# Kernel optimization log

Hardware: AMD Instinct MI355X
Metric: run time of the kernel (lower is better)

Reference implementation:

```python
import jax, jax.numpy as jnp
import numpy as np

T, B, E, H = 2048, 2, 1024, 16
D = E // H  # head_dim = 64

def setup_inputs() -> dict:
    key = jax.random.key(0)
    ks = jax.random.split(key, 9)
    s = 1.0 / np.sqrt(E)
    return {
        "query": jax.random.normal(ks[0], (T, B, E), dtype=jnp.float32),
        "Wq": jax.random.normal(ks[1], (E, E), dtype=jnp.float32) * s,
        "bq": jax.random.normal(ks[2], (E,), dtype=jnp.float32) * 0.02,
        "Wk": jax.random.normal(ks[3], (E, E), dtype=jnp.float32) * s,
        "bk": jax.random.normal(ks[4], (E,), dtype=jnp.float32) * 0.02,
        "Wv": jax.random.normal(ks[5], (E, E), dtype=jnp.float32) * s,
        "bv": jax.random.normal(ks[6], (E,), dtype=jnp.float32) * 0.02,
        "Wo": jax.random.normal(ks[7], (E, E), dtype=jnp.float32) * s,
        "bo": jax.random.normal(ks[8], (E,), dtype=jnp.float32) * 0.02,
    }

def reference(query, Wq, bq, Wk, bk, Wv, bv, Wo, bo):
    # query: [T, B, E] (fairseq Time x Batch x Channel layout)
    t, b, e = query.shape
    scaling = D ** -0.5
    q = (query @ Wq.T + bq) * scaling          # [T,B,E], scaled like fairseq
    k = query @ Wk.T + bk                      # self-attention: k,v from query
    v = query @ Wv.T + bv
    # split heads: [T,B,H,D]
    q = q.reshape(t, b, H, D)
    k = k.reshape(t, b, H, D)
    v = v.reshape(t, b, H, D)
    # attn weights: [B,H,T(tgt),S(src)]
    scores = jnp.einsum("tbhd,sbhd->bhts", q, k)
    probs = jax.nn.softmax(scores, axis=-1)
    # attend: [T,B,H,D] -> [T,B,E]
    ctx = jnp.einsum("bhts,sbhd->tbhd", probs, v).reshape(t, b, e)
    return ctx @ Wo.T + bo                     # [T,B,E]
```

## Files before the change

kernel.cpp:

```cpp
#include <hip/hip_runtime.h>
#include <hip/hip_bf16.h>
#include <math.h>

#define TT 2048
#define BB 2
#define EE 1024
#define HH 16
#define DD 64
#define RR (TT*BB)

typedef __bf16 bf16x8 __attribute__((ext_vector_type(8)));
typedef float  floatx4 __attribute__((ext_vector_type(4)));

__device__ __forceinline__ unsigned short f2b(float f) {
    union { float f; unsigned u; } x{f};
    return (unsigned short)((x.u + 0x7FFFu + ((x.u >> 16) & 1u)) >> 16);
}
__device__ __forceinline__ float b2f_lo(unsigned u) {
    union { unsigned u; float f; } x{u << 16}; return x.f;
}
__device__ __forceinline__ float b2f_hi(unsigned u) {
    union { unsigned u; float f; } x{u & 0xffff0000u}; return x.f;
}

__device__ __forceinline__ float exp2_fast(float x) {
    return __builtin_amdgcn_exp2f(x);
}

typedef const __attribute__((address_space(1))) unsigned int as1_u32;
typedef __attribute__((address_space(3))) unsigned int as3_u32;
__device__ __forceinline__ void gload16(const void* g, void* l) {
    __builtin_amdgcn_global_load_lds((as1_u32*)g, (as3_u32*)l, 16, 0, 0);
}

#define SCALE_Q 0.18033688011112042f

__device__ __forceinline__ int swz(int r) {
    return (r & 7) ^ (((r >> 3) & 3) << 1);
}

__global__ __launch_bounds__(256)
void pack_bf16(const float* __restrict__ x,  const float* __restrict__ wq,
               const float* __restrict__ wk, const float* __restrict__ wv,
               const float* __restrict__ wo, unsigned short* __restrict__ base,
               unsigned short* __restrict__ wob)
{
    const size_t M4 = (size_t)4 << 20, M7 = (size_t)7 << 20;
    const size_t e0 = ((size_t)blockIdx.x * 256 + threadIdx.x) * 8;
    const float* src;
    unsigned short* dst;
    if (e0 < M4) {
        src = x + e0; dst = base + e0;
    } else if (e0 < M7) {
        const int seg = (int)((e0 >> 20) - 4);
        const float* wsrc[3] = {wq, wk, wv};
        src = wsrc[seg] + (e0 & ((1u << 20) - 1));
        dst = base + e0;
    } else {
        src = wo + (e0 - M7); dst = wob + (e0 - M7);
    }
    const float4 a = *(const float4*)src;
    const float4 b = *(const float4*)(src + 4);
    union { unsigned short u[8]; uint4 v; } p;
    p.u[0] = f2b(a.x); p.u[1] = f2b(a.y); p.u[2] = f2b(a.z); p.u[3] = f2b(a.w);
    p.u[4] = f2b(b.x); p.u[5] = f2b(b.y); p.u[6] = f2b(b.z); p.u[7] = f2b(b.w);
    *(uint4*)dst = p.v;
}

template<int MODE>
__global__ __launch_bounds__(256)
void gemm_mfma(const unsigned short* __restrict__ A,
               const unsigned short* __restrict__ Bw,
               const float* __restrict__ b0, const float* __restrict__ b1,
               const float* __restrict__ b2,
               void* __restrict__ out0, void* __restrict__ out1,
               void* __restrict__ out2)
{
    constexpr int BM = 128;
    constexpr int BN = (MODE == 0) ? 128 : 64;
    constexpr int MT = 4;
    constexpr int NT = (MODE == 0) ? 4 : 2;
    constexpr int RA = BM / 32;
    constexpr int RB = BN / 32;
    constexpr int ABYTES = BM * 128;
    constexpr int BUFB   = (BM + BN) * 128;
    __shared__ __align__(16) unsigned char smem[2 * BUFB];

    const int tid  = threadIdx.x;
    const int w    = tid >> 6;
    const int lane = tid & 63;
    const int quad = lane >> 4;
    const int l15  = lane & 15;
    const int wm   = w & 1;
    const int wn   = w >> 1;
    const int i0   = blockIdx.x * BM;
    const int j0   = blockIdx.y * BN;

    const unsigned short* ga[RA];
    const unsigned short* gb[RB];
    #pragma unroll
    for (int r = 0; r < RA; ++r) {
        const int slot = r * 256 + tid;
        const int row  = slot >> 3;
        const int gc   = (slot & 7) ^ swz(row);
        ga[r] = A + (size_t)(i0 + row) * EE + gc * 8;
    }
    #pragma unroll
    for (int r = 0; r < RB; ++r) {
        const int slot = r * 256 + tid;
        const int row  = slot >> 3;
        const int gc   = (slot & 7) ^ swz(row);
        gb[r] = Bw + (size_t)(j0 + row) * EE + gc * 8;
    }

    int ofsA[2][MT], ofsB[2][NT];
    #pragma unroll
    for (int mt = 0; mt < MT; ++mt) {
        const int row = wm * 64 + mt * 16 + l15;
        #pragma unroll
        for (int ks = 0; ks < 2; ++ks)
            ofsA[ks][mt] = row * 64 + (((ks * 4 + quad) ^ swz(row)) << 3);
    }
    #pragma unroll
    for (int nt = 0; nt < NT; ++nt) {
        const int col = wn * (BN / 2) + nt * 16 + l15;
        #pragma unroll
        for (int ks = 0; ks < 2; ++ks)
            ofsB[ks][nt] = col * 64 + (((ks * 4 + quad) ^ swz(col)) << 3);
    }

    floatx4 acc[MT][NT];
    #pragma unroll
    for (int mt = 0; mt < MT; ++mt)
        #pragma unroll
        for (int nt = 0; nt < NT; ++nt)
            acc[mt][nt] = (floatx4){0.f, 0.f, 0.f, 0.f};

    {
        unsigned short* nA = (unsigned short*)(smem);
        unsigned short* nB = (unsigned short*)(smem + ABYTES);
        #pragma unroll
        for (int r = 0; r < RA; ++r)
            gload16(ga[r], nA + (r * 256 + w * 64) * 8);
        #pragma unroll
        for (int r = 0; r < RB; ++r)
            gload16(gb[r], nB + (r * 256 + w * 64) * 8);
    }

    int cur = 0;
    for (int kk = 0; kk < EE; kk += 64) {
        __syncthreads();

        const unsigned short* lA = (const unsigned short*)(smem + cur * BUFB);
        const unsigned short* lB = (const unsigned short*)(smem + cur * BUFB + ABYTES);

        bf16x8 af[2][MT], bfr[2][NT];
        #pragma unroll
        for (int ks = 0; ks < 2; ++ks) {
            #pragma unroll
            for (int mt = 0; mt < MT; ++mt)
                af[ks][mt] = __builtin_bit_cast(bf16x8, *(const uint4*)&lA[ofsA[ks][mt]]);
            #pragma unroll
            for (int nt = 0; nt < NT; ++nt)
                bfr[ks][nt] = __builtin_bit_cast(bf16x8, *(const uint4*)&lB[ofsB[ks][nt]]);
        }

        if (kk + 64 < EE) {
            const int nxt = cur ^ 1;
            unsigned short* nA = (unsigned short*)(smem + nxt * BUFB);
            unsigned short* nB = (unsigned short*)(smem + nxt * BUFB + ABYTES);
            #pragma unroll
            for (int r = 0; r < RA; ++r)
                gload16(ga[r] + kk + 64, nA + (r * 256 + w * 64) * 8);
            #pragma unroll
            for (int r = 0; r < RB; ++r)
                gload16(gb[r] + kk + 64, nB + (r * 256 + w * 64) * 8);
        }
        __builtin_amdgcn_sched_barrier(0);

        #pragma unroll
        for (int ks = 0; ks < 2; ++ks)
            #pragma unroll
            for (int mt = 0; mt < MT; ++mt)
                #pragma unroll
                for (int nt = 0; nt < NT; ++nt)
                    acc[mt][nt] = __builtin_amdgcn_mfma_f32_16x16x32_bf16(
                        af[ks][mt], bfr[ks][nt], acc[mt][nt], 0, 0, 0);

        cur ^= 1;
    }

    if (MODE == 1) {
        float* dst = (float*)out0;
        #pragma unroll
        for (int nt = 0; nt < NT; ++nt) {
            const int j = j0 + wn * 32 + nt * 16 + l15;
            const float bb = b0[j];
            #pragma unroll
            for (int mt = 0; mt < MT; ++mt) {
                const int i = i0 + wm * 64 + mt * 16 + quad * 4;
                #pragma unroll
                for (int r2 = 0; r2 < 4; ++r2)
                    dst[(size_t)(i + r2) * EE + j] = acc[mt][nt][r2] + bb;
            }
        }
    } else {
        const int which = j0 >> 10;
        const float scale = (which == 0) ? SCALE_Q : 1.0f;
        const float* bias = (which == 0) ? b0 : (which == 1) ? b1 : b2;
        if (which < 2) {
            unsigned short* dst = (unsigned short*)(which == 0 ? out0 : out1);
            #pragma unroll
            for (int nt = 0; nt < NT; ++nt) {
                const int j = (j0 & 1023) + wn * 64 + nt * 16 + l15;
                const int h = j >> 6, d = j & 63;
                const float bb = bias[j];
                #pragma unroll
                for (int mt = 0; mt < MT; ++mt) {
                    const int i = i0 + wm * 64 + mt * 16 + quad * 4;
                    #pragma unroll
                    for (int r2 = 0; r2 < 4; ++r2) {
                        const int ii = i + r2;
                        const int t = ii >> 1, b = ii & 1;
                        dst[((size_t)(b * HH + h) * TT + t) * DD + d] =
                            f2b((acc[mt][nt][r2] + bb) * scale);
                    }
                }
            }
        } else {
            __syncthreads();
            unsigned short* tr = (unsigned short*)smem + (size_t)w * 64 * 68;
            #pragma unroll
            for (int nt = 0; nt < NT; ++nt) {
                const int jl = nt * 16 + l15;
                const float bb = bias[(j0 & 1023) + wn * 64 + jl];
                #pragma unroll
                for (int mt = 0; mt < MT; ++mt) {
                    const int il0 = mt * 16 + quad * 4;
                    ushort4 h4;
                    h4.x = f2b(acc[mt][nt][0] + bb);
                    h4.y = f2b(acc[mt][nt][1] + bb);
                    h4.z = f2b(acc[mt][nt][2] + bb);
                    h4.w = f2b(acc[mt][nt][3] + bb);
                    *(ushort4*)&tr[jl * 68 + il0] = h4;
                }
            }
            __syncthreads();
            const int jg = (j0 & 1023) + wn * 64 + lane;
            const int h = jg >> 6, d = jg & 63;
            const int tb = (i0 + wm * 64) >> 1;
            const unsigned short* rp = tr + (size_t)lane * 68;
            unsigned short* dstV = (unsigned short*)out2;
            #pragma unroll
            for (int g = 0; g < 4; ++g) {
                union { unsigned short u[8]; uint4 v; } pe, po;
                #pragma unroll
                for (int k = 0; k < 8; ++k) {
                    pe.u[k] = rp[(g * 8 + k) * 2];
                    po.u[k] = rp[(g * 8 + k) * 2 + 1];
                }
                *(uint4*)&dstV[((size_t)(0 * HH + h) * DD + d) * TT + tb + g * 8] = pe.v;
                *(uint4*)&dstV[((size_t)(1 * HH + h) * DD + d) * TT + tb + g * 8] = po.v;
            }
        }
    }
}

__global__ __launch_bounds__(256)
void attn_mfma(const unsigned short* __restrict__ Q,
               const unsigned short* __restrict__ K,
               const unsigned short* __restrict__ Vt,
               unsigned short* __restrict__ cpart,
               float* __restrict__ lsumbuf)
{
    __shared__ __align__(16) unsigned short ksm[2][64 * 64];
    __shared__ __align__(16) unsigned short vtm[2][64 * 64];

    const int tid  = threadIdx.x;
    const int w    = tid >> 6;
    const int lane = tid & 63;
    const int quad = lane >> 4;
    const int l15  = lane & 15;
    const int bh   = blockIdx.x;
    const int tt   = blockIdx.y;
    const int half = blockIdx.z;

    const unsigned short* Qh = Q  + (size_t)bh * TT * DD;
    const unsigned short* Kh = K  + (size_t)bh * TT * DD;
    const unsigned short* Vh = Vt + (size_t)bh * DD * TT;

    const int q0w  = tt * 128 + w * 32;
    const int key0 = half * 1024;

    bf16x8 qf[2][2];
    #pragma unroll
    for (int qn = 0; qn < 2; ++qn)
        #pragma unroll
        for (int kd = 0; kd < 2; ++kd)
            qf[qn][kd] = __builtin_bit_cast(bf16x8,
                *(const uint4*)&Qh[(size_t)(q0w + qn * 16 + l15) * DD + kd * 32 + quad * 8]);

    const unsigned short* kg[4];
    #pragma unroll
    for (int r = 0; r < 4; ++r) {
        const int slot = r * 256 + tid;
        const int row  = slot >> 3;
        const int gc   = (slot & 7) ^ swz(row);
        kg[r] = Kh + (size_t)(key0 + row) * DD + gc * 8;
    }
    const unsigned short* vg[4];
    #pragma unroll
    for (int r = 0; r < 4; ++r) {
        const int s512 = (r & 1) * 256 + tid;
        const int rowd = s512 >> 3;
        const int gc   = (s512 & 7) ^ swz(rowd);
        vg[r] = Vh + (size_t)rowd * TT + key0 + (r >> 1) * 64 + gc * 8;
    }

    int ofsKA[4][2], ofsVB[4][2];
    #pragma unroll
    for (int mt = 0; mt < 4; ++mt) {
        const int row = ((mt >> 1) << 5) + ((l15 >> 2) << 3) + ((mt & 1) << 2) + (l15 & 3);
        #pragma unroll
        for (int kd = 0; kd < 2; ++kd)
            ofsKA[mt][kd] = row * 64 + (((kd * 4 + quad) ^ swz(row)) << 3);
    }
    #pragma unroll
    for (int dn = 0; dn < 4; ++dn) {
        const int row = dn * 16 + l15;
        #pragma unroll
        for (int ks = 0; ks < 2; ++ks)
            ofsVB[dn][ks] = row * 64 + (((ks * 4 + quad) ^ swz(row)) << 3);
    }

    floatx4 cacc[4][2];
    #pragma unroll
    for (int dn = 0; dn < 4; ++dn)
        #pragma unroll
        for (int qn = 0; qn < 2; ++qn)
            cacc[dn][qn] = (floatx4){0.f, 0.f, 0.f, 0.f};
    float rs[2] = {0.f, 0.f};

    for (int big = 0; big < 8; ++big) {
        const size_t ko = (size_t)big * 128;
        __syncthreads();
        gload16(kg[0] + ko * DD, &ksm[0][(size_t)(0 * 256 + w * 64) * 8]);
        gload16(kg[1] + ko * DD, &ksm[0][(size_t)(1 * 256 + w * 64) * 8]);
        gload16(kg[2] + ko * DD, &ksm[1][(size_t)(0 * 256 + w * 64) * 8]);
        gload16(kg[3] + ko * DD, &ksm[1][(size_t)(1 * 256 + w * 64) * 8]);
        gload16(vg[0] + ko,      &vtm[0][(size_t)(0 * 256 + w * 64) * 8]);
        gload16(vg[1] + ko,      &vtm[0][(size_t)(1 * 256 + w * 64) * 8]);
        gload16(vg[2] + ko,      &vtm[1][(size_t)(0 * 256 + w * 64) * 8]);
        gload16(vg[3] + ko,      &vtm[1][(size_t)(1 * 256 + w * 64) * 8]);
        __syncthreads();

        #pragma unroll
        for (int sub = 0; sub < 2; ++sub) {
            uint2 pk[4][2];
            #pragma unroll
            for (int mt = 0; mt < 4; ++mt) {
                const bf16x8 ka0 = __builtin_bit_cast(bf16x8, *(const uint4*)&ksm[sub][ofsKA[mt][0]]);
                const bf16x8 ka1 = __builtin_bit_cast(bf16x8, *(const uint4*)&ksm[sub][ofsKA[mt][1]]);
                #pragma unroll
                for (int qn = 0; qn < 2; ++qn) {
                    floatx4 s = (floatx4){0.f, 0.f, 0.f, 0.f};
                    s = __builtin_amdgcn_mfma_f32_16x16x32_bf16(ka0, qf[qn][0], s, 0, 0, 0);
                    s = __builtin_amdgcn_mfma_f32_16x16x32_bf16(ka1, qf[qn][1], s, 0, 0, 0);
                    const float p0 = exp2_fast(s[0]);
                    const float p1 = exp2_fast(s[1]);
                    const float p2 = exp2_fast(s[2]);
                    const float p3 = exp2_fast(s[3]);
                    rs[qn] += (p0 + p1) + (p2 + p3);
                    union { __hip_bfloat162 h2[2]; uint2 u; } c;
                    c.h2[0] = __float22bfloat162_rn(make_float2(p0, p1));
                    c.h2[1] = __float22bfloat162_rn(make_float2(p2, p3));
                    pk[mt][qn] = c.u;
                }
            }
            bf16x8 pa[2][2];
            #pragma unroll
            for (int qn = 0; qn < 2; ++qn) {
                union { uint2 d[2]; uint4 v; } a0, a1;
                a0.d[0] = pk[0][qn]; a0.d[1] = pk[1][qn];
                a1.d[0] = pk[2][qn]; a1.d[1] = pk[3][qn];
                pa[qn][0] = __builtin_bit_cast(bf16x8, a0.v);
                pa[qn][1] = __builtin_bit_cast(bf16x8, a1.v);
            }
            #pragma unroll
            for (int dn = 0; dn < 4; ++dn) {
                const bf16x8 vb0 = __builtin_bit_cast(bf16x8, *(const uint4*)&vtm[sub][ofsVB[dn][0]]);
                const bf16x8 vb1 = __builtin_bit_cast(bf16x8, *(const uint4*)&vtm[sub][ofsVB[dn][1]]);
                #pragma unroll
                for (int qn = 0; qn < 2; ++qn) {
                    cacc[dn][qn] = __builtin_amdgcn_mfma_f32_16x16x32_bf16(pa[qn][0], vb0, cacc[dn][qn], 0, 0, 0);
                    cacc[dn][qn] = __builtin_amdgcn_mfma_f32_16x16x32_bf16(pa[qn][1], vb1, cacc[dn][qn], 0, 0, 0);
                }
            }
        }
    }

    const int b = bh / HH, hh = bh % HH;
    float rsw[2];
    #pragma unroll
    for (int qn = 0; qn < 2; ++qn) {
        float t = rs[qn];
        t += __shfl_xor(t, 16);
        t += __shfl_xor(t, 32);
        rsw[qn] = t;
    }
    unsigned short* cp = cpart + (size_t)half * RR * EE;
    #pragma unroll
    for (int qn = 0; qn < 2; ++qn) {
        #pragma unroll
        for (int dn = 0; dn < 4; ++dn) {
            const int e = hh * 64 + dn * 16 + l15;
            #pragma unroll
            for (int j = 0; j < 4; ++j) {
                const int t = q0w + qn * 16 + quad * 4 + j;
                cp[(size_t)(t * BB + b) * EE + e] = f2b(cacc[dn][qn][j]);
            }
        }
    }
    if (quad == 0) {
        lsumbuf[(half * BB * HH + bh) * TT + q0w + 0 * 16 + l15] = rsw[0];
        lsumbuf[(half * BB * HH + bh) * TT + q0w + 1 * 16 + l15] = rsw[1];
    }
}

__global__ __launch_bounds__(256)
void combine(const unsigned short* __restrict__ cpart,
             const float* __restrict__ lsumbuf,
             unsigned short* __restrict__ cb)
{
    const int gid = blockIdx.x * 256 + threadIdx.x;
    const int e0 = (gid & 127) * 8;
    const int r  = gid >> 7;
    const int t = r >> 1, b = r & 1;
    const int h = e0 >> 6;
    const int bh = b * HH + h;
    const float inv = 1.0f /
        (lsumbuf[bh * TT + t] + lsumbuf[(BB * HH + bh) * TT + t]);
    const uint4 c0 = *(const uint4*)&cpart[(size_t)r * EE + e0];
    const uint4 c1 = *(const uint4*)&cpart[(size_t)RR * EE + (size_t)r * EE + e0];
    const unsigned u0[4] = {c0.x, c0.y, c0.z, c0.w};
    const unsigned u1[4] = {c1.x, c1.y, c1.z, c1.w};
    union { unsigned u[4]; uint4 v; } o;
    #pragma unroll
    for (int k = 0; k < 4; ++k) {
        const float lo = (b2f_lo(u0[k]) + b2f_lo(u1[k])) * inv;
        const float hi = (b2f_hi(u0[k]) + b2f_hi(u1[k])) * inv;
        union { __hip_bfloat162 h2; unsigned u; } pk;
        pk.h2 = __float22bfloat162_rn(make_float2(lo, hi));
        o.u[k] = pk.u;
    }
    *(uint4*)&cb[(size_t)r * EE + e0] = o.v;
}

extern "C" void kernel_launch(void* const* d_in, const int* in_sizes, int n_in,
                              void* d_out, int out_size, void* d_ws, size_t ws_size,
                              hipStream_t stream)
{
    const float* x  = (const float*)d_in[0];
    const float* Wq = (const float*)d_in[1];
    const float* bq = (const float*)d_in[2];
    const float* Wk = (const float*)d_in[3];
    const float* bk = (const float*)d_in[4];
    const float* Wv = (const float*)d_in[5];
    const float* bv = (const float*)d_in[6];
    const float* Wo = (const float*)d_in[7];
    const float* bo = (const float*)d_in[8];
    float* out = (float*)d_out;

    const size_t M1 = (size_t)1 << 20;
    unsigned short* base  = (unsigned short*)d_ws;
    unsigned short* xb    = base;
    unsigned short* wqkv  = base + 4 * M1;
    unsigned short* cpart = base;
    unsigned short* qb    = base + 8 * M1;
    unsigned short* kb    = base + 12 * M1;
    unsigned short* vtb   = base + 16 * M1;
    unsigned short* cb    = base + 20 * M1;
    unsigned short* wob   = base + 24 * M1;
    float*          lsum  = (float*)(base + 25 * M1);

    dim3 blk(256);

    pack_bf16<<<dim3(4096), blk, 0, stream>>>(x, Wq, Wk, Wv, Wo, base, wob);

    gemm_mfma<0><<<dim3(RR / 128, 3072 / 128), blk, 0, stream>>>(
        xb, wqkv, bq, bk, bv, qb, kb, vtb);

    attn_mfma<<<dim3(BB * HH, TT / 128, 2), blk, 0, stream>>>(qb, kb, vtb, cpart, lsum);

    combine<<<dim3(RR * EE / 8 / 256), blk, 0, stream>>>(cpart, lsum, cb);

    gemm_mfma<1><<<dim3(RR / 128, EE / 64), blk, 0, stream>>>(
        cb, wob, bo, nullptr, nullptr, out, nullptr, nullptr);
}
```

Measured before the change: 189.5 us.

## Pipeline attention K/V loads with a three-stage LDS ring and reorder GEMM prefetch

The attention kernel previously loaded each 128-key K/V chunk synchronously between two barriers, so global-to-LDS latency was fully exposed. It now uses a three-buffer LDS ring with 64-key stages, issuing loads two stages ahead and waiting with vmcnt-based partial waits before one barrier per step. The GEMM loop also moves its next-tile prefetch ahead of the LDS fragment reads, using an explicit vmcnt(0) wait plus s_barrier. The ring raises LDS use by half, which may lower occupancy, and the hand-counted vmcnt values depend on gload16 issuing exactly one memory op each.

Result: faster. 179.7 us (-5.2%).

```diff
diff --git a/kernel.cpp b/kernel.cpp
--- a/kernel.cpp
+++ b/kernel.cpp
@@ -149,7 +149,20 @@
 
     int cur = 0;
     for (int kk = 0; kk < EE; kk += 64) {
-        __syncthreads();
+        asm volatile("s_waitcnt vmcnt(0)" ::: "memory");
+        __builtin_amdgcn_s_barrier();
+
+        if (kk + 64 < EE) {
+            unsigned short* nA = (unsigned short*)(smem + (cur ^ 1) * BUFB);
+            unsigned short* nB = (unsigned short*)(smem + (cur ^ 1) * BUFB + ABYTES);
+            #pragma unroll
+            for (int r = 0; r < RA; ++r)
+                gload16(ga[r] + kk + 64, nA + (r * 256 + w * 64) * 8);
+            #pragma unroll
+            for (int r = 0; r < RB; ++r)
+                gload16(gb[r] + kk + 64, nB + (r * 256 + w * 64) * 8);
+        }
+        __builtin_amdgcn_sched_barrier(0);
 
         const unsigned short* lA = (const unsigned short*)(smem + cur * BUFB);
         const unsigned short* lB = (const unsigned short*)(smem + cur * BUFB + ABYTES);
@@ -164,19 +177,6 @@
             for (int nt = 0; nt < NT; ++nt)
                 bfr[ks][nt] = __builtin_bit_cast(bf16x8, *(const uint4*)&lB[ofsB[ks][nt]]);
         }
-
-        if (kk + 64 < EE) {
-            const int nxt = cur ^ 1;
-            unsigned short* nA = (unsigned short*)(smem + nxt * BUFB);
-            unsigned short* nB = (unsigned short*)(smem + nxt * BUFB + ABYTES);
-            #pragma unroll
-            for (int r = 0; r < RA; ++r)
-                gload16(ga[r] + kk + 64, nA + (r * 256 + w * 64) * 8);
-            #pragma unroll
-            for (int r = 0; r < RB; ++r)
-                gload16(gb[r] + kk + 64, nB + (r * 256 + w * 64) * 8);
-        }
-        __builtin_amdgcn_sched_barrier(0);
 
         #pragma unroll
         for (int ks = 0; ks < 2; ++ks)
@@ -273,8 +273,7 @@
                unsigned short* __restrict__ cpart,
                float* __restrict__ lsumbuf)
 {
-    __shared__ __align__(16) unsigned short ksm[2][64 * 64];
-    __shared__ __align__(16) unsigned short vtm[2][64 * 64];
+    __shared__ __align__(16) unsigned short ring[3][2][64 * 64];
 
     const int tid  = threadIdx.x;
     const int w    = tid >> 6;
@@ -341,63 +340,74 @@
             cacc[dn][qn] = (floatx4){0.f, 0.f, 0.f, 0.f};
     float rs[2] = {0.f, 0.f};
 
-    for (int big = 0; big < 8; ++big) {
-        const size_t ko = (size_t)big * 128;
-        __syncthreads();
-        gload16(kg[0] + ko * DD, &ksm[0][(size_t)(0 * 256 + w * 64) * 8]);
-        gload16(kg[1] + ko * DD, &ksm[0][(size_t)(1 * 256 + w * 64) * 8]);
-        gload16(kg[2] + ko * DD, &ksm[1][(size_t)(0 * 256 + w * 64) * 8]);
-        gload16(kg[3] + ko * DD, &ksm[1][(size_t)(1 * 256 + w * 64) * 8]);
-        gload16(vg[0] + ko,      &vtm[0][(size_t)(0 * 256 + w * 64) * 8]);
-        gload16(vg[1] + ko,      &vtm[0][(size_t)(1 * 256 + w * 64) * 8]);
-        gload16(vg[2] + ko,      &vtm[1][(size_t)(0 * 256 + w * 64) * 8]);
-        gload16(vg[3] + ko,      &vtm[1][(size_t)(1 * 256 + w * 64) * 8]);
-        __syncthreads();
-
-        #pragma unroll
-        for (int sub = 0; sub < 2; ++sub) {
-            uint2 pk[4][2];
-            #pragma unroll
-            for (int mt = 0; mt < 4; ++mt) {
-                const bf16x8 ka0 = __builtin_bit_cast(bf16x8, *(const uint4*)&ksm[sub][ofsKA[mt][0]]);
-                const bf16x8 ka1 = __builtin_bit_cast(bf16x8, *(const uint4*)&ksm[sub][ofsKA[mt][1]]);
-                #pragma unroll
-                for (int qn = 0; qn < 2; ++qn) {
-                    floatx4 s = (floatx4){0.f, 0.f, 0.f, 0.f};
-                    s = __builtin_amdgcn_mfma_f32_16x16x32_bf16(ka0, qf[qn][0], s, 0, 0, 0);
-                    s = __builtin_amdgcn_mfma_f32_16x16x32_bf16(ka1, qf[qn][1], s, 0, 0, 0);
-                    const float p0 = exp2_fast(s[0]);
-                    const float p1 = exp2_fast(s[1]);
-                    const float p2 = exp2_fast(s[2]);
-                    const float p3 = exp2_fast(s[3]);
-                    rs[qn] += (p0 + p1) + (p2 + p3);
-                    union { __hip_bfloat162 h2[2]; uint2 u; } c;
-                    c.h2[0] = __float22bfloat162_rn(make_float2(p0, p1));
-                    c.h2[1] = __float22bfloat162_rn(make_float2(p2, p3));
-                    pk[mt][qn] = c.u;
-                }
-            }
-            bf16x8 pa[2][2];
+#define STAGE_ATTN(s)  do {                                                     \
+        const int p_ = (s) & 1;                                                 \
+        const size_t ko_ = (size_t)((s) >> 1) * 128;                            \
+        unsigned short* kd_ = &ring[(s) % 3][0][0];                             \
+        unsigned short* vd_ = &ring[(s) % 3][1][0];                             \
+        gload16(kg[2 * p_]     + ko_ * DD, kd_ + (size_t)(0 * 256 + w * 64) * 8); \
+        gload16(kg[2 * p_ + 1] + ko_ * DD, kd_ + (size_t)(1 * 256 + w * 64) * 8); \
+        gload16(vg[2 * p_]     + ko_,      vd_ + (size_t)(0 * 256 + w * 64) * 8); \
+        gload16(vg[2 * p_ + 1] + ko_,      vd_ + (size_t)(1 * 256 + w * 64) * 8); \
+    } while (0)
+
+    STAGE_ATTN(0);
+    STAGE_ATTN(1);
+
+    #pragma unroll
+    for (int step = 0; step < 16; ++step) {
+        const int rb = step % 3;
+        if (step < 15) asm volatile("s_waitcnt vmcnt(4)" ::: "memory");
+        else           asm volatile("s_waitcnt vmcnt(0)" ::: "memory");
+        __builtin_amdgcn_s_barrier();
+        if (step + 2 < 16) STAGE_ATTN(step + 2);
+        __builtin_amdgcn_sched_barrier(0);
+
+        const unsigned short* ksub = &ring[rb][0][0];
+        const unsigned short* vsub = &ring[rb][1][0];
+
+        uint2 pk[4][2];
+        #pragma unroll
+        for (int mt = 0; mt < 4; ++mt) {
+            const bf16x8 ka0 = __builtin_bit_cast(bf16x8, *(const uint4*)&ksub[ofsKA[mt][0]]);
+            const bf16x8 ka1 = __builtin_bit_cast(bf16x8, *(const uint4*)&ksub[ofsKA[mt][1]]);
             #pragma unroll
             for (int qn = 0; qn < 2; ++qn) {
-                union { uint2 d[2]; uint4 v; } a0, a1;
-                a0.d[0] = pk[0][qn]; a0.d[1] = pk[1][qn];
-                a1.d[0] = pk[2][qn]; a1.d[1] = pk[3][qn];
-                pa[qn][0] = __builtin_bit_cast(bf16x8, a0.v);
-                pa[qn][1] = __builtin_bit_cast(bf16x8, a1.v);
-            }
-            #pragma unroll
-            for (int dn = 0; dn < 4; ++dn) {
-                const bf16x8 vb0 = __builtin_bit_cast(bf16x8, *(const uint4*)&vtm[sub][ofsVB[dn][0]]);
-                const bf16x8 vb1 = __builtin_bit_cast(bf16x8, *(const uint4*)&vtm[sub][ofsVB[dn][1]]);
-                #pragma unroll
-                for (int qn = 0; qn < 2; ++qn) {
-                    cacc[dn][qn] = __builtin_amdgcn_mfma_f32_16x16x32_bf16(pa[qn][0], vb0, cacc[dn][qn], 0, 0, 0);
-                    cacc[dn][qn] = __builtin_amdgcn_mfma_f32_16x16x32_bf16(pa[qn][1], vb1, cacc[dn][qn], 0, 0, 0);
-                }
-            }
-        }
-    }
+                floatx4 s = (floatx4){0.f, 0.f, 0.f, 0.f};
+                s = __builtin_amdgcn_mfma_f32_16x16x32_bf16(ka0, qf[qn][0], s, 0, 0, 0);
+                s = __builtin_amdgcn_mfma_f32_16x16x32_bf16(ka1, qf[qn][1], s, 0, 0, 0);
+                const float p0 = exp2_fast(s[0]);
+                const float p1 = exp2_fast(s[1]);
+                const float p2 = exp2_fast(s[2]);
+                const float p3 = exp2_fast(s[3]);
+                rs[qn] += (p0 + p1) + (p2 + p3);
+                union { __hip_bfloat162 h2[2]; uint2 u; } c;
+                c.h2[0] = __float22bfloat162_rn(make_float2(p0, p1));
+                c.h2[1] = __float22bfloat162_rn(make_float2(p2, p3));
+                pk[mt][qn] = c.u;
+            }
+        }
+        bf16x8 pa[2][2];
+        #pragma unroll
+        for (int qn = 0; qn < 2; ++qn) {
+            union { uint2 d[2]; uint4 v; } a0, a1;
+            a0.d[0] = pk[0][qn]; a0.d[1] = pk[1][qn];
+            a1.d[0] = pk[2][qn]; a1.d[1] = pk[3][qn];
+            pa[qn][0] = __builtin_bit_cast(bf16x8, a0.v);
+            pa[qn][1] = __builtin_bit_cast(bf16x8, a1.v);
+        }
+        #pragma unroll
+        for (int dn = 0; dn < 4; ++dn) {
+            const bf16x8 vb0 = __builtin_bit_cast(bf16x8, *(const uint4*)&vsub[ofsVB[dn][0]]);
+            const bf16x8 vb1 = __builtin_bit_cast(bf16x8, *(const uint4*)&vsub[ofsVB[dn][1]]);
+            #pragma unroll
+            for (int qn = 0; qn < 2; ++qn) {
+                cacc[dn][qn] = __builtin_amdgcn_mfma_f32_16x16x32_bf16(pa[qn][0], vb0, cacc[dn][qn], 0, 0, 0);
+                cacc[dn][qn] = __builtin_amdgcn_mfma_f32_16x16x32_bf16(pa[qn][1], vb1, cacc[dn][qn], 0, 0, 0);
+            }
+        }
+    }
+#undef STAGE_ATTN
 
     const int b = bh / HH, hh = bh % HH;
     float rsw[2];
```
